# Kernel tuning notes

Measured on AMD Instinct MI355X. Metric: run time of the kernel, lower is better.

## Reference

```python
import jax, jax.numpy as jnp
import numpy as np

B, L, T = 512, 512, 128
START, STOP = T - 2, T - 1   # tag_dict: '<START>'->126, '<STOP>'->127
NEG = -10000.0


def setup_inputs() -> dict:
    key = jax.random.key(0)
    k1, k2, k3, k4 = jax.random.split(key, 4)
    feats = jax.random.normal(k1, (B, L, T), dtype=jnp.float32)
    # learned transition matrix, initialized as in CRF.__init__
    trans = jax.random.normal(k2, (T, T), dtype=jnp.float32)
    trans = trans.at[START, :].set(NEG).at[:, STOP].set(NEG)
    tags = jax.random.randint(k3, (B, L), 0, T - 2)          # gold tags, no START/STOP
    lens = jax.random.randint(k4, (B,), 1, L + 1)            # actual lengths in [1, L]
    return {"feats": feats, "transitions": trans, "tags": tags, "lens": lens}


def _crf_loss(feats, transitions, tags, lens):
    Bn, Ln, Tn = feats.shape

    # ---- forward algorithm (log partition) ----
    init = jnp.full((Tn,), NEG, dtype=feats.dtype).at[START].set(0.0)
    fv0 = jnp.broadcast_to(init, (Bn, Tn))

    def step(fv, xs):
        emit, i = xs                                  # emit: [B, T]
        # tag_var[b, next, prev] = emit[b,next] + trans[next,prev] + fv[b,prev]
        tv = emit[:, :, None] + transitions[None, :, :] + fv[:, None, :]
        new = jax.scipy.special.logsumexp(tv, axis=2)  # [B, T]
        # freeze fv once past each sentence's length (== gathering at index lens)
        fv = jnp.where((i < lens)[:, None], new, fv)
        return fv, None

    fv, _ = jax.lax.scan(step, fv0, (jnp.swapaxes(feats, 0, 1), jnp.arange(Ln)))
    terminal = fv + transitions[START][None, :]       # matches original (uses START row)
    forward_score = jax.scipy.special.logsumexp(terminal, axis=1)  # [B]

    # ---- gold sentence score ----
    start_col = jnp.full((Bn, 1), START, dtype=tags.dtype)
    stop_col = jnp.full((Bn, 1), STOP, dtype=tags.dtype)
    pad_start = jnp.concatenate([start_col, tags], axis=1)   # [B, L+1]
    pad_stop = jnp.concatenate([tags, stop_col], axis=1)     # [B, L+1]
    pos = jnp.arange(Ln + 1)[None, :]
    pad_stop = jnp.where(pos >= lens[:, None], STOP, pad_stop)

    trans_terms = transitions[pad_stop, pad_start]           # [B, L+1]
    trans_sum = jnp.sum(jnp.where(pos <= lens[:, None], trans_terms, 0.0), axis=1)
    emit_terms = jnp.take_along_axis(feats, tags[:, :, None], axis=2)[..., 0]  # [B, L]
    emit_mask = jnp.arange(Ln)[None, :] < lens[:, None]
    emit_sum = jnp.sum(jnp.where(emit_mask, emit_terms, 0.0), axis=1)
    gold_score = trans_sum + emit_sum

    return jnp.mean(forward_score - gold_score)


def reference(feats, transitions, tags, lens):
    return _crf_loss(feats, transitions, tags, lens)
```

## Files before the change

### kernel.cpp

```cpp
#include <hip/hip_runtime.h>

#define Bsz 512
#define Lsz 512
#define Tsz 128
#define TAG_START 126
#define TAG_STOP 127
#define SPB 16
#define UPITCH 136

typedef __attribute__((ext_vector_type(8))) short short8;
typedef __attribute__((ext_vector_type(4))) float f32x4;

__device__ __forceinline__ void lds_barrier() {
  asm volatile("s_waitcnt lgkmcnt(0)\n\ts_barrier" ::: "memory");
}
__device__ __forceinline__ unsigned pack_bf16(float lo, float hi) {
  unsigned a = (__float_as_uint(lo) + 0x8000u) >> 16;
  unsigned b = (__float_as_uint(hi) + 0x8000u) & 0xFFFF0000u;
  return b | a;
}
__device__ __forceinline__ float bf16lo(unsigned d) { return __uint_as_float(d << 16); }
__device__ __forceinline__ float bf16hi(unsigned d) { return __uint_as_float(d & 0xFFFF0000u); }

__global__ __launch_bounds__(256) void crf_fwd_kernel(
    const float* __restrict__ feats, const float* __restrict__ trans,
    const int* __restrict__ tags, const int* __restrict__ lens,
    float* __restrict__ diff_out)
{
  __shared__ __align__(16) unsigned short u_lds[2][SPB][UPITCH];
  __shared__ float red[4][SPB];
  __shared__ float gold_sh[SPB];
  __shared__ int msh;

  const int g    = blockIdx.x;
  const int tid  = threadIdx.x;
  const int w    = tid >> 6;
  const int lane = tid & 63;
  const int q    = lane >> 4;
  const int s    = lane & 15;
  const int seq  = g * SPB + s;
  const int lenc = lens[seq];

  if (tid == 0) msh = 1;
  __syncthreads();
  if (tid < SPB) atomicMax(&msh, lens[g * SPB + tid]);
  for (int i = tid; i < 2 * SPB * UPITCH; i += 256)
    ((unsigned short*)u_lds)[i] = 0;
  __syncthreads();
  const int maxlen = msh;
  if (tid < SPB) u_lds[0][tid][TAG_START] = 0x3F80;
  __syncthreads();

  short8 af[2][4];
  #pragma unroll
  for (int i = 0; i < 2; ++i) {
    const float* tr = trans + (size_t)((2 * w + i) * 16 + s) * Tsz + q * 8;
    #pragma unroll
    for (int c = 0; c < 4; ++c) {
      float4 x = *(const float4*)(tr + c * 32);
      float4 y = *(const float4*)(tr + c * 32 + 4);
      union { unsigned u[4]; short8 v; } cv;
      cv.u[0] = pack_bf16(__expf(x.x), __expf(x.y));
      cv.u[1] = pack_bf16(__expf(x.z), __expf(x.w));
      cv.u[2] = pack_bf16(__expf(y.x), __expf(y.y));
      cv.u[3] = pack_bf16(__expf(y.z), __expf(y.w));
      af[i][c] = cv.v;
    }
  }

  unsigned off0[8];
  #pragma unroll
  for (int i = 0; i < 2; ++i)
    #pragma unroll
    for (int r = 0; r < 4; ++r)
      off0[i * 4 + r] = (unsigned)seq * (Lsz * Tsz) + (2 * w + i) * 16 + 4 * q + r;

  float pfa[8], pfb[8];
  { int t1 = (1 < maxlen) ? 1 : 0;
    #pragma unroll
    for (int i = 0; i < 8; ++i) pfa[i] = feats[off0[i]];
    #pragma unroll
    for (int i = 0; i < 8; ++i) pfb[i] = feats[off0[i] + (unsigned)t1 * Tsz]; }

  float m_run = 0.0f, mcap = 0.0f;
  float ucap[8];
  #pragma unroll
  for (int i = 0; i < 8; ++i) ucap[i] = 1.0f;

#define STEP(T, PF, BR, BW)                                                    \
  { const int t_ = (T);                                                        \
    short8 bq0 = *(const short8*)&u_lds[BR][s][0 * 32 + q * 8];                \
    short8 bq1 = *(const short8*)&u_lds[BR][s][1 * 32 + q * 8];                \
    short8 bq2 = *(const short8*)&u_lds[BR][s][2 * 32 + q * 8];                \
    short8 bq3 = *(const short8*)&u_lds[BR][s][3 * 32 + q * 8];                \
    unsigned ud = *(const unsigned*)&u_lds[BR][s][0];                          \
    float eta = bf16lo(ud) + bf16hi(ud);                                       \
    if (t_ == 0) eta = 1.0f;                                                   \
    float ee[8];                                                               \
    _Pragma("unroll") for (int i = 0; i < 8; ++i) ee[i] = __expf(PF[i]);       \
    f32x4 acc0 = {0.f, 0.f, 0.f, 0.f}, acc1 = {0.f, 0.f, 0.f, 0.f};            \
    acc0 = __builtin_amdgcn_mfma_f32_16x16x32_bf16(af[0][0], bq0, acc0, 0,0,0);\
    acc1 = __builtin_amdgcn_mfma_f32_16x16x32_bf16(af[1][0], bq0, acc1, 0,0,0);\
    acc0 = __builtin_amdgcn_mfma_f32_16x16x32_bf16(af[0][1], bq1, acc0, 0,0,0);\
    acc1 = __builtin_amdgcn_mfma_f32_16x16x32_bf16(af[1][1], bq1, acc1, 0,0,0);\
    acc0 = __builtin_amdgcn_mfma_f32_16x16x32_bf16(af[0][2], bq2, acc0, 0,0,0);\
    acc1 = __builtin_amdgcn_mfma_f32_16x16x32_bf16(af[1][2], bq2, acc1, 0,0,0);\
    acc0 = __builtin_amdgcn_mfma_f32_16x16x32_bf16(af[0][3], bq3, acc0, 0,0,0);\
    acc1 = __builtin_amdgcn_mfma_f32_16x16x32_bf16(af[1][3], bq3, acc1, 0,0,0);\
    int tp = t_ + 2; if (tp >= maxlen) tp = maxlen - 1;                        \
    unsigned toff = (unsigned)tp * Tsz;                                        \
    _Pragma("unroll") for (int i = 0; i < 8; ++i) PF[i] = feats[off0[i] + toff];\
    float rce = __builtin_amdgcn_rcpf(eta);                                    \
    bool capt = (t_ == lenc - 1);                                              \
    float uv[8];                                                               \
    _Pragma("unroll") for (int i = 0; i < 4; ++i) {                            \
      uv[i]     = acc0[i] * rce * ee[i];                                       \
      uv[4 + i] = acc1[i] * rce * ee[4 + i];                                   \
    }                                                                          \
    _Pragma("unroll") for (int i = 0; i < 8; ++i)                              \
      ucap[i] = capt ? uv[i] : ucap[i];                                        \
    m_run += __logf(eta);                                                      \
    mcap = capt ? m_run : mcap;                                                \
    unsigned short* dst = &u_lds[BW][s][0];                                    \
    *(unsigned*)&dst[(2 * w + 0) * 16 + 4 * q]     = pack_bf16(uv[0], uv[1]);  \
    *(unsigned*)&dst[(2 * w + 0) * 16 + 4 * q + 2] = pack_bf16(uv[2], uv[3]);  \
    *(unsigned*)&dst[(2 * w + 1) * 16 + 4 * q]     = pack_bf16(uv[4], uv[5]);  \
    *(unsigned*)&dst[(2 * w + 1) * 16 + 4 * q + 2] = pack_bf16(uv[6], uv[7]);  \
    lds_barrier();                                                             \
  }

  for (int t = 0; t < maxlen; t += 2) {
    STEP(t, pfa, 0, 1)
    if (t + 1 < maxlen) STEP(t + 1, pfb, 1, 0)
  }
#undef STEP

  __syncthreads();

  float fvv[8];
  #pragma unroll
  for (int i = 0; i < 2; ++i)
    #pragma unroll
    for (int r = 0; r < 4; ++r) {
      int row = (2 * w + i) * 16 + 4 * q + r;
      fvv[i * 4 + r] = __logf(ucap[i * 4 + r]) + mcap + trans[TAG_START * Tsz + row];
    }
  float mx = fvv[0];
  #pragma unroll
  for (int i = 1; i < 8; ++i) mx = fmaxf(mx, fvv[i]);
  mx = fmaxf(mx, __shfl_xor(mx, 16, 64));
  mx = fmaxf(mx, __shfl_xor(mx, 32, 64));
  if (q == 0) red[w][s] = mx;
  __syncthreads();
  float gmx = fmaxf(fmaxf(red[0][s], red[1][s]), fmaxf(red[2][s], red[3][s]));
  __syncthreads();
  float se = 0.f;
  #pragma unroll
  for (int i = 0; i < 8; ++i) se += __expf(fvv[i] - gmx);
  se += __shfl_xor(se, 16, 64);
  se += __shfl_xor(se, 32, 64);
  if (q == 0) red[w][s] = se;
  __syncthreads();
  float fwd_score = gmx + __logf((red[0][s] + red[1][s]) + (red[2][s] + red[3][s]));

  {
    int jj = 4 * w + q;
    int gs2 = g * SPB + jj;
    int lenj = lens[gs2];
    const int* tg = tags + (size_t)gs2 * Lsz;
    const float* fbj = feats + (size_t)gs2 * (Lsz * Tsz);
    float acc = 0.f;
    for (int pos = s; pos <= lenj; pos += 16) {
      int st = (pos == 0)    ? TAG_START : tg[pos - 1];
      int et = (pos == lenj) ? TAG_STOP  : tg[pos];
      acc += trans[et * Tsz + st];
    }
    for (int l = s; l < lenj; l += 16)
      acc += fbj[(size_t)l * Tsz + tg[l]];
    #pragma unroll
    for (int off = 1; off < 16; off <<= 1) acc += __shfl_xor(acc, off, 64);
    if (s == 0) gold_sh[jj] = acc;
  }
  __syncthreads();
  if (w == 0 && q == 0)
    diff_out[g * SPB + s] = fwd_score - gold_sh[s];
}

__global__ __launch_bounds__(Bsz) void crf_final_kernel(
    const float* __restrict__ diff, float* __restrict__ out)
{
  int tid = threadIdx.x;
  float v = diff[tid];
  __shared__ float wred[8];
  float sum = v;
  #pragma unroll
  for (int off = 32; off > 0; off >>= 1) sum += __shfl_down(sum, off, 64);
  int wave = tid >> 6, lane = tid & 63;
  if (lane == 0) wred[wave] = sum;
  __syncthreads();
  if (tid == 0) {
    float t = 0.f;
    #pragma unroll
    for (int i = 0; i < 8; ++i) t += wred[i];
    out[0] = t * (1.0f / Bsz);
  }
}

extern "C" void kernel_launch(void* const* d_in, const int* in_sizes, int n_in,
                              void* d_out, int out_size, void* d_ws, size_t ws_size,
                              hipStream_t stream) {
  const float* feats = (const float*)d_in[0];
  const float* trans = (const float*)d_in[1];
  const int*   tags  = (const int*)d_in[2];
  const int*   lens  = (const int*)d_in[3];
  float* out  = (float*)d_out;
  float* diff = (float*)d_ws;

  crf_fwd_kernel<<<Bsz / SPB, 256, 0, stream>>>(feats, trans, tags, lens, diff);
  crf_final_kernel<<<1, Bsz, 0, stream>>>(diff, out);
}
```

Baseline: 449.4 us.

## Deepen feats prefetch to four steps with float4 loads and early exp

The per-step emission loads become two float4 loads per lane instead of eight scalar loads. The prefetch distance grows from two to four timesteps, clamped to each sequence's own length. The exp of the next step's emissions now runs before the barrier, so it leaves the dependency chain at the top of each step. The loop is unrolled by four without tail guards, so up to three extra steps may run past maxlen; their results are discarded, but they add some wasted work and register pressure.

```diff
diff --git a/kernel.cpp b/kernel.cpp
--- a/kernel.cpp
+++ b/kernel.cpp
@@ -40,6 +40,7 @@
   const int s    = lane & 15;
   const int seq  = g * SPB + s;
   const int lenc = lens[seq];
+  const int lim  = lenc - 1;
 
   if (tid == 0) msh = 1;
   __syncthreads();
@@ -68,36 +69,35 @@
     }
   }
 
-  unsigned off0[8];
-  #pragma unroll
-  for (int i = 0; i < 2; ++i)
-    #pragma unroll
-    for (int r = 0; r < 4; ++r)
-      off0[i * 4 + r] = (unsigned)seq * (Lsz * Tsz) + (2 * w + i) * 16 + 4 * q + r;
-
-  float pfa[8], pfb[8];
-  { int t1 = (1 < maxlen) ? 1 : 0;
-    #pragma unroll
-    for (int i = 0; i < 8; ++i) pfa[i] = feats[off0[i]];
-    #pragma unroll
-    for (int i = 0; i < 8; ++i) pfb[i] = feats[off0[i] + (unsigned)t1 * Tsz]; }
+  const float* fp0 = feats + (size_t)seq * (Lsz * Tsz) + (2 * w + 0) * 16 + 4 * q;
+  const float* fp1 = feats + (size_t)seq * (Lsz * Tsz) + (2 * w + 1) * 16 + 4 * q;
+
+  float4 pa0, pb0, pa1, pb1, pa2, pb2, pa3, pb3;
+  { int r1 = (1 < lim) ? 1 : lim, r2 = (2 < lim) ? 2 : lim, r3 = (3 < lim) ? 3 : lim;
+    if (lim < 1) r1 = r2 = r3 = lim;
+    pa0 = *(const float4*)(fp0);                       pb0 = *(const float4*)(fp1);
+    pa1 = *(const float4*)(fp0 + ((size_t)r1 << 7));   pb1 = *(const float4*)(fp1 + ((size_t)r1 << 7));
+    pa2 = *(const float4*)(fp0 + ((size_t)r2 << 7));   pb2 = *(const float4*)(fp1 + ((size_t)r2 << 7));
+    pa3 = *(const float4*)(fp0 + ((size_t)r3 << 7));   pb3 = *(const float4*)(fp1 + ((size_t)r3 << 7)); }
+
+  float ee[8] = {__expf(pa0.x), __expf(pa0.y), __expf(pa0.z), __expf(pa0.w),
+                 __expf(pb0.x), __expf(pb0.y), __expf(pb0.z), __expf(pb0.w)};
 
   float m_run = 0.0f, mcap = 0.0f;
   float ucap[8];
   #pragma unroll
   for (int i = 0; i < 8; ++i) ucap[i] = 1.0f;
 
-#define STEP(T, PF, BR, BW)                                                    \
+#define STEP(T, PA, PB, NA, NB, BR, BW)                                        \
   { const int t_ = (T);                                                        \
     short8 bq0 = *(const short8*)&u_lds[BR][s][0 * 32 + q * 8];                \
     short8 bq1 = *(const short8*)&u_lds[BR][s][1 * 32 + q * 8];                \
     short8 bq2 = *(const short8*)&u_lds[BR][s][2 * 32 + q * 8];                \
     short8 bq3 = *(const short8*)&u_lds[BR][s][3 * 32 + q * 8];                \
     unsigned ud = *(const unsigned*)&u_lds[BR][s][0];                          \
-    float eta = bf16lo(ud) + bf16hi(ud);                                       \
-    if (t_ == 0) eta = 1.0f;                                                   \
-    float ee[8];                                                               \
-    _Pragma("unroll") for (int i = 0; i < 8; ++i) ee[i] = __expf(PF[i]);       \
+    int tp = t_ + 4; tp = (tp < lim) ? tp : lim;                               \
+    PA = *(const float4*)(fp0 + ((size_t)tp << 7));                            \
+    PB = *(const float4*)(fp1 + ((size_t)tp << 7));                            \
     f32x4 acc0 = {0.f, 0.f, 0.f, 0.f}, acc1 = {0.f, 0.f, 0.f, 0.f};            \
     acc0 = __builtin_amdgcn_mfma_f32_16x16x32_bf16(af[0][0], bq0, acc0, 0,0,0);\
     acc1 = __builtin_amdgcn_mfma_f32_16x16x32_bf16(af[1][0], bq0, acc1, 0,0,0);\
@@ -107,11 +107,10 @@
     acc1 = __builtin_amdgcn_mfma_f32_16x16x32_bf16(af[1][2], bq2, acc1, 0,0,0);\
     acc0 = __builtin_amdgcn_mfma_f32_16x16x32_bf16(af[0][3], bq3, acc0, 0,0,0);\
     acc1 = __builtin_amdgcn_mfma_f32_16x16x32_bf16(af[1][3], bq3, acc1, 0,0,0);\
-    int tp = t_ + 2; if (tp >= maxlen) tp = maxlen - 1;                        \
-    unsigned toff = (unsigned)tp * Tsz;                                        \
-    _Pragma("unroll") for (int i = 0; i < 8; ++i) PF[i] = feats[off0[i] + toff];\
+    float eta = bf16lo(ud) + bf16hi(ud);                                       \
+    if (t_ == 0) eta = 1.0f;                                                   \
     float rce = __builtin_amdgcn_rcpf(eta);                                    \
-    bool capt = (t_ == lenc - 1);                                              \
+    bool capt = (t_ == lim);                                                   \
     float uv[8];                                                               \
     _Pragma("unroll") for (int i = 0; i < 4; ++i) {                            \
       uv[i]     = acc0[i] * rce * ee[i];                                       \
@@ -126,12 +125,18 @@
     *(unsigned*)&dst[(2 * w + 0) * 16 + 4 * q + 2] = pack_bf16(uv[2], uv[3]);  \
     *(unsigned*)&dst[(2 * w + 1) * 16 + 4 * q]     = pack_bf16(uv[4], uv[5]);  \
     *(unsigned*)&dst[(2 * w + 1) * 16 + 4 * q + 2] = pack_bf16(uv[6], uv[7]);  \
+    ee[0] = __expf(NA.x); ee[1] = __expf(NA.y);                                \
+    ee[2] = __expf(NA.z); ee[3] = __expf(NA.w);                                \
+    ee[4] = __expf(NB.x); ee[5] = __expf(NB.y);                                \
+    ee[6] = __expf(NB.z); ee[7] = __expf(NB.w);                                \
     lds_barrier();                                                             \
   }
 
-  for (int t = 0; t < maxlen; t += 2) {
-    STEP(t, pfa, 0, 1)
-    if (t + 1 < maxlen) STEP(t + 1, pfb, 1, 0)
+  for (int t = 0; t < maxlen; t += 4) {
+    STEP(t + 0, pa0, pb0, pa1, pb1, 0, 1)
+    STEP(t + 1, pa1, pb1, pa2, pb2, 1, 0)
+    STEP(t + 2, pa2, pb2, pa3, pb3, 0, 1)
+    STEP(t + 3, pa3, pb3, pa0, pb0, 1, 0)
   }
 #undef STEP
 
```

Measured after the change: 407.2 us. 1.1x faster.
